# Optimization experiments

Hardware: AMD Instinct MI355X
Metric: run time of the kernel (lower is better)

Reference implementation:

```python
import jax, jax.numpy as jnp
import numpy as np

D_MODEL = 1024
N_HEADS = 16
D_HEAD = D_MODEL // N_HEADS


def setup_inputs() -> dict:
    key = jax.random.key(0)
    ks = jax.random.split(key, 9)
    s = 1.0 / np.sqrt(D_MODEL)
    x = jax.random.normal(ks[0], (2, 2048, D_MODEL), dtype=jnp.float32)
    Wq = jax.random.uniform(ks[1], (D_MODEL, D_MODEL), jnp.float32, -s, s)
    bq = jax.random.uniform(ks[2], (D_MODEL,), jnp.float32, -s, s)
    Wk = jax.random.uniform(ks[3], (D_MODEL, D_MODEL), jnp.float32, -s, s)
    bk = jax.random.uniform(ks[4], (D_MODEL,), jnp.float32, -s, s)
    Wv = jax.random.uniform(ks[5], (D_MODEL, D_MODEL), jnp.float32, -s, s)
    bv = jax.random.uniform(ks[6], (D_MODEL,), jnp.float32, -s, s)
    Wo = jax.random.uniform(ks[7], (D_MODEL, D_MODEL), jnp.float32, -s, s)
    bo = jax.random.uniform(ks[8], (D_MODEL,), jnp.float32, -s, s)
    return {"x": x, "Wq": Wq, "bq": bq, "Wk": Wk, "bk": bk,
            "Wv": Wv, "bv": bv, "Wo": Wo, "bo": bo}


def reference(x, Wq, bq, Wk, bk, Wv, bv, Wo, bo):
    B, T, _ = x.shape
    # projections: (B, T, d_model) -> (B, H, T, d_head)
    def split_heads(y):
        return y.reshape(B, T, N_HEADS, D_HEAD).transpose(0, 2, 1, 3)
    Q = split_heads(x @ Wq + bq)
    K = split_heads(x @ Wk + bk)
    V = split_heads(x @ Wv + bv)
    scores = jnp.einsum('bhqd,bhkd->bhqk', Q, K) / jnp.sqrt(jnp.float32(D_HEAD))
    causal = jnp.tril(jnp.ones((T, T), dtype=bool))  # allowed positions
    scores = jnp.where(causal, scores, -jnp.inf)
    attn = jax.nn.softmax(scores, axis=-1)
    out = jnp.einsum('bhqk,bhkd->bhqd', attn, V)
    out = out.transpose(0, 2, 1, 3).reshape(B, T, D_MODEL)
    return out @ Wo + bo
```

## Files before the change

kernel.cpp:

```cpp
#include <hip/hip_runtime.h>

typedef unsigned short u16;
typedef unsigned int u32;

#define DM 1024
#define NH 16
#define DH 64
#define BB 2
#define TT 2048

#define SCLQ 0.18033688f

using frag8  = __attribute__((ext_vector_type(8))) short;
using bf16x8 = __attribute__((ext_vector_type(8))) __bf16;
using f32x4  = __attribute__((ext_vector_type(4))) float;

__device__ inline u16 f2bf(float f) {
  union { float f; u32 u; } v; v.f = f;
  u32 r = v.u + 0x7fffu + ((v.u >> 16) & 1u);
  return (u16)(r >> 16);
}

__device__ inline f32x4 mfma_bf16(frag8 a, frag8 b, f32x4 c) {
  return __builtin_amdgcn_mfma_f32_16x16x32_bf16(
      __builtin_bit_cast(bf16x8, a), __builtin_bit_cast(bf16x8, b), c, 0, 0, 0);
}

__device__ inline void gld16(void* lds, const void* g) {
  __builtin_amdgcn_global_load_lds(
      (const __attribute__((address_space(1))) void*)g,
      (__attribute__((address_space(3))) void*)lds, 16, 0, 0);
}

__device__ inline int swi(int row, int chunk) {
  return row * 64 + ((chunk ^ (row & 7)) << 3);
}

__global__ __launch_bounds__(256) void cvt_x_kernel(const float* __restrict__ X,
                                                    u16* __restrict__ Y) {
  int i = blockIdx.x * 256 + threadIdx.x;
  float4 v = ((const float4*)X)[i];
  ushort4 o;
  o.x = f2bf(v.x); o.y = f2bf(v.y); o.z = f2bf(v.z); o.w = f2bf(v.w);
  ((ushort4*)Y)[i] = o;
}

__global__ __launch_bounds__(256) void transpose_w_kernel(
    const float* __restrict__ W0, const float* __restrict__ W1,
    const float* __restrict__ W2, const float* __restrict__ W3,
    u16* __restrict__ O0, u16* __restrict__ O1,
    u16* __restrict__ O2, u16* __restrict__ O3) {
  const float* W; u16* Ot;
  switch (blockIdx.z) {
    case 0: W = W0; Ot = O0; break;
    case 1: W = W1; Ot = O1; break;
    case 2: W = W2; Ot = O2; break;
    default: W = W3; Ot = O3; break;
  }
  __shared__ u16 Ls[64][72];
  int tid = threadIdx.x;
  int n0 = blockIdx.x * 64;
  int k0 = blockIdx.y * 64;
#pragma unroll
  for (int p = 0; p < 4; ++p) {
    int id = tid + p * 256;
    int row = id >> 4;
    int c4 = (id & 15) * 4;
    float4 v = *(const float4*)&W[(size_t)(k0 + row) * DM + n0 + c4];
    ushort4 o; o.x = f2bf(v.x); o.y = f2bf(v.y); o.z = f2bf(v.z); o.w = f2bf(v.w);
    *(ushort4*)&Ls[row][c4] = o;
  }
  __syncthreads();
#pragma unroll
  for (int p = 0; p < 4; ++p) {
    int id = tid + p * 256;
    int row = id >> 4;
    int c4 = (id & 15) * 4;
    ushort4 o;
    o.x = Ls[c4 + 0][row]; o.y = Ls[c4 + 1][row];
    o.z = Ls[c4 + 2][row]; o.w = Ls[c4 + 3][row];
    *(ushort4*)&Ot[(size_t)(n0 + row) * DM + k0 + c4] = o;
  }
}

__global__ __launch_bounds__(256, 3) void gemm_qkv_kernel(
    const u16* __restrict__ A, const u16* __restrict__ Bt,
    const float* __restrict__ b0, const float* __restrict__ b1,
    const float* __restrict__ b2,
    u16* __restrict__ QK, u16* __restrict__ Vb) {
  constexpr int K = 1024;
  __shared__ u16 As[2][4096];
  __shared__ u16 Bs[2][4096];
  int tid = threadIdx.x;
  int lane = tid & 63, w = tid >> 6;
  int qd = lane >> 4, ln = lane & 15;
  int wm = (w & 1) * 64, wn = (w >> 1) * 64;
  int m0 = blockIdx.y * 128, n0 = blockIdx.x * 128;
  f32x4 z = {0.f, 0.f, 0.f, 0.f};
  f32x4 acc[4][4];
#pragma unroll
  for (int mi = 0; mi < 4; ++mi)
#pragma unroll
    for (int ni = 0; ni < 4; ++ni) acc[mi][ni] = z;

  const u16* ga = A + (size_t)(m0 + w * 32 + (lane >> 2)) * K + (lane & 3) * 8;
  const u16* gb = Bt + (size_t)(n0 + w * 32 + (lane >> 2)) * K + (lane & 3) * 8;

  gld16(&As[0][w * 1024],       ga);
  gld16(&As[0][w * 1024 + 512], ga + 16 * K);
  gld16(&Bs[0][w * 1024],       gb);
  gld16(&Bs[0][w * 1024 + 512], gb + 16 * K);

  for (int k0 = 0; k0 < K; k0 += 32) {
    int cur = (k0 >> 5) & 1;
    __syncthreads();
    if (k0 + 32 < K) {
      int nb = cur ^ 1;
      gld16(&As[nb][w * 1024],       ga + k0 + 32);
      gld16(&As[nb][w * 1024 + 512], ga + k0 + 32 + 16 * K);
      gld16(&Bs[nb][w * 1024],       gb + k0 + 32);
      gld16(&Bs[nb][w * 1024 + 512], gb + k0 + 32 + 16 * K);
    }
    frag8 af[4], bfr[4];
#pragma unroll
    for (int mi = 0; mi < 4; ++mi)
      af[mi] = *(const frag8*)&As[cur][(wm + mi * 16 + ln) * 32 + qd * 8];
#pragma unroll
    for (int ni = 0; ni < 4; ++ni)
      bfr[ni] = *(const frag8*)&Bs[cur][(wn + ni * 16 + ln) * 32 + qd * 8];
#pragma unroll
    for (int mi = 0; mi < 4; ++mi)
#pragma unroll
      for (int ni = 0; ni < 4; ++ni)
        acc[mi][ni] = mfma_bf16(af[mi], bfr[ni], acc[mi][ni]);
  }

#pragma unroll
  for (int ni = 0; ni < 4; ++ni) {
    int col = n0 + wn + ni * 16 + ln;
    if (col < 2048) {
      bool isq = col < 1024;
      float bias = isq ? b0[col] : b1[col - 1024];
#pragma unroll
      for (int mi = 0; mi < 4; ++mi) {
        int row = m0 + wm + mi * 16 + qd * 4;
#pragma unroll
        for (int r = 0; r < 4; ++r) {
          float v = acc[mi][ni][r] + bias;
          if (isq) v *= SCLQ;
          QK[(size_t)(row + r) * 2048 + col] = f2bf(v);
        }
      }
    } else {
      int c2 = col - 2048;
      float bias = b2[c2];
#pragma unroll
      for (int mi = 0; mi < 4; ++mi) {
        int row = m0 + wm + mi * 16 + qd * 4;
#pragma unroll
        for (int r = 0; r < 4; ++r)
          Vb[(size_t)(row + r) * 1024 + c2] = f2bf(acc[mi][ni][r] + bias);
      }
    }
  }
}

__global__ __launch_bounds__(256) void gemm_out_kernel(
    const u16* __restrict__ A, const u16* __restrict__ Bt,
    const float* __restrict__ b0, float* __restrict__ Cf) {
  constexpr int K = 1024;
  __shared__ u16 As[2][4096];
  __shared__ u16 Bs[2][2048];
  int tid = threadIdx.x;
  int lane = tid & 63, w = tid >> 6;
  int qd = lane >> 4, ln = lane & 15;
  int m0 = blockIdx.y * 128, n0 = blockIdx.x * 64;
  f32x4 z = {0.f, 0.f, 0.f, 0.f};
  f32x4 acc[2][4];
#pragma unroll
  for (int mi = 0; mi < 2; ++mi)
#pragma unroll
    for (int ni = 0; ni < 4; ++ni) acc[mi][ni] = z;

  const u16* ga = A + (size_t)(m0 + w * 32 + (lane >> 2)) * K + (lane & 3) * 8;
  const u16* gb = Bt + (size_t)(n0 + w * 16 + (lane >> 2)) * K + (lane & 3) * 8;

  gld16(&As[0][w * 1024],       ga);
  gld16(&As[0][w * 1024 + 512], ga + 16 * K);
  gld16(&Bs[0][w * 512],        gb);

  for (int k0 = 0; k0 < K; k0 += 32) {
    int cur = (k0 >> 5) & 1;
    __syncthreads();
    if (k0 + 32 < K) {
      int nb = cur ^ 1;
      gld16(&As[nb][w * 1024],       ga + k0 + 32);
      gld16(&As[nb][w * 1024 + 512], ga + k0 + 32 + 16 * K);
      gld16(&Bs[nb][w * 512],        gb + k0 + 32);
    }
    frag8 af[2], bfr[4];
#pragma unroll
    for (int mi = 0; mi < 2; ++mi)
      af[mi] = *(const frag8*)&As[cur][(w * 32 + mi * 16 + ln) * 32 + qd * 8];
#pragma unroll
    for (int ni = 0; ni < 4; ++ni)
      bfr[ni] = *(const frag8*)&Bs[cur][(ni * 16 + ln) * 32 + qd * 8];
#pragma unroll
    for (int mi = 0; mi < 2; ++mi)
#pragma unroll
      for (int ni = 0; ni < 4; ++ni)
        acc[mi][ni] = mfma_bf16(af[mi], bfr[ni], acc[mi][ni]);
  }

#pragma unroll
  for (int ni = 0; ni < 4; ++ni) {
    int col = n0 + ni * 16 + ln;
    float bias = b0[col];
#pragma unroll
    for (int mi = 0; mi < 2; ++mi) {
      int row = m0 + w * 32 + mi * 16 + qd * 4;
#pragma unroll
      for (int r = 0; r < 4; ++r)
        Cf[(size_t)(row + r) * 1024 + col] = acc[mi][ni][r] + bias;
    }
  }
}

__global__ __launch_bounds__(256) void transpose_v_kernel(const u16* __restrict__ V,
                                                          u16* __restrict__ Vt) {
  int bh = blockIdx.y;
  int b = bh >> 4, h = bh & 15;
  int t0 = blockIdx.x * 64;
  __shared__ u16 Ls[64][72];
  int tid = threadIdx.x;
#pragma unroll
  for (int p = 0; p < 2; ++p) {
    int id = tid + p * 256;
    int row = id >> 3, seg = id & 7;
    *(uint4*)&Ls[row][seg * 8] =
        *(const uint4*)&V[(size_t)(b * TT + t0 + row) * DM + h * DH + seg * 8];
  }
  __syncthreads();
#pragma unroll
  for (int p = 0; p < 2; ++p) {
    int id = tid + p * 256;
    int d = id >> 3, seg = id & 7;
    union { u16 s[8]; uint4 v; } tmp;
#pragma unroll
    for (int j = 0; j < 8; ++j) tmp.s[j] = Ls[seg * 8 + j][d];
    *(uint4*)&Vt[(size_t)(bh * DH + d) * TT + t0 + seg * 8] = tmp.v;
  }
}

__global__ __launch_bounds__(256, 4) void flash5_kernel(const u16* __restrict__ QK,
                                                        const u16* __restrict__ Vt,
                                                        u16* __restrict__ O) {
  int qt = blockIdx.x;
  int bh = blockIdx.y;
  int b = bh >> 4, h = bh & 15;
  int q0 = qt * 64;
  __shared__ u16 Ks[2 * 4096];
  __shared__ u16 Vs[2 * 4096];
  __shared__ u16 Ps[4096];
  int tid = threadIdx.x;
  int lane = tid & 63, w = tid >> 6;
  int qd = lane >> 4, ln = lane & 15;

  frag8 qf[2];
#pragma unroll
  for (int kk = 0; kk < 2; ++kk)
    qf[kk] = *(const frag8*)&QK[(size_t)(b * TT + q0 + w * 16 + ln) * 2048 +
                                h * 64 + kk * 32 + qd * 8];

  int lr = lane >> 3, lc = (lane & 7) ^ lr;
  const u16* Kg  = &QK[(size_t)(b * TT + w * 16 + lr) * 2048 + 1024 + h * 64 + lc * 8];
  const u16* Kg2 = Kg + 8 * 2048;
  const u16* Vg  = &Vt[(size_t)(bh * 64 + w * 16 + lr) * 2048 + lc * 8];
  const u16* Vg2 = Vg + 8 * 2048;
  int ldsw = w * 1024;

  int nkt = qt + 1;

  gld16(&Ks[ldsw],       Kg);
  gld16(&Ks[ldsw + 512], Kg2);
  gld16(&Vs[ldsw],       Vg);
  gld16(&Vs[ldsw + 512], Vg2);

  float l = 0.f;
  f32x4 z = {0.f, 0.f, 0.f, 0.f};
  f32x4 o[4] = {z, z, z, z};

  for (int kt = 0; kt < nkt; ++kt) {
    int cur = kt & 1;
    int cb = cur * 4096;
    __syncthreads();

    if (kt + 1 < nkt) {
      int nb = (cur ^ 1) * 4096;
      size_t ko = (size_t)(kt + 1) * 64 * 2048;
      int vo = (kt + 1) * 64;
      gld16(&Ks[nb + ldsw],       Kg + ko);
      gld16(&Ks[nb + ldsw + 512], Kg2 + ko);
      gld16(&Vs[nb + ldsw],       Vg + vo);
      gld16(&Vs[nb + ldsw + 512], Vg2 + vo);
    }

    bool diag = (kt == qt);

    f32x4 s[4] = {z, z, z, z};
    __builtin_amdgcn_s_setprio(1);
#pragma unroll
    for (int mi = 0; mi < 4; ++mi) {
      if (diag && mi > w) continue;
#pragma unroll
      for (int kk = 0; kk < 2; ++kk) {
        frag8 ak = *(const frag8*)&Ks[cb + swi(mi * 16 + ln, 4 * kk + qd)];
        s[mi] = mfma_bf16(ak, qf[kk], s[mi]);
      }
    }
    __builtin_amdgcn_s_setprio(0);

#pragma unroll
    for (int mi = 0; mi < 4; ++mi) {
      int pb = swi(w * 16 + ln, 2 * mi + (qd >> 1)) + (qd & 1) * 4;
      if (diag && mi > w) {
        uint2 zz; zz.x = 0u; zz.y = 0u;
        *(uint2*)&Ps[pb] = zz;
        continue;
      }
      float p0 = __builtin_amdgcn_exp2f(s[mi][0]);
      float p1 = __builtin_amdgcn_exp2f(s[mi][1]);
      float p2 = __builtin_amdgcn_exp2f(s[mi][2]);
      float p3 = __builtin_amdgcn_exp2f(s[mi][3]);
      if (diag && mi == w) {
        p0 = (qd * 4 + 0 <= ln) ? p0 : 0.f;
        p1 = (qd * 4 + 1 <= ln) ? p1 : 0.f;
        p2 = (qd * 4 + 2 <= ln) ? p2 : 0.f;
        p3 = (qd * 4 + 3 <= ln) ? p3 : 0.f;
      }
      l += (p0 + p1) + (p2 + p3);
      u32 u0 = __builtin_bit_cast(u32, p0) + 0x8000u;
      u32 u1 = __builtin_bit_cast(u32, p1) + 0x8000u;
      u32 u2 = __builtin_bit_cast(u32, p2) + 0x8000u;
      u32 u3 = __builtin_bit_cast(u32, p3) + 0x8000u;
      uint2 pk;
      pk.x = __builtin_amdgcn_perm(u1, u0, 0x07060302u);
      pk.y = __builtin_amdgcn_perm(u3, u2, 0x07060302u);
      *(uint2*)&Ps[pb] = pk;
    }

    __builtin_amdgcn_s_setprio(1);
#pragma unroll
    for (int kk = 0; kk < 2; ++kk) {
      if (diag && kk == 1 && w < 2) continue;
      frag8 bp = *(const frag8*)&Ps[swi(w * 16 + ln, 4 * kk + qd)];
#pragma unroll
      for (int mi = 0; mi < 4; ++mi) {
        frag8 av = *(const frag8*)&Vs[cb + swi(mi * 16 + ln, 4 * kk + qd)];
        o[mi] = mfma_bf16(av, bp, o[mi]);
      }
    }
    __builtin_amdgcn_s_setprio(0);
  }

  l += __shfl_xor(l, 16);
  l += __shfl_xor(l, 32);
  float rl = 1.0f / l;

#pragma unroll
  for (int mi = 0; mi < 4; ++mi) {
    ushort4 ov;
    ov.x = f2bf(o[mi][0] * rl); ov.y = f2bf(o[mi][1] * rl);
    ov.z = f2bf(o[mi][2] * rl); ov.w = f2bf(o[mi][3] * rl);
    *(ushort4*)&O[(size_t)(b * TT + q0 + w * 16 + ln) * DM + h * 64 + mi * 16 + qd * 4] = ov;
  }
}

extern "C" void kernel_launch(void* const* d_in, const int* in_sizes, int n_in,
                              void* d_out, int out_size, void* d_ws, size_t ws_size,
                              hipStream_t stream) {
  const float* x  = (const float*)d_in[0];
  const float* Wq = (const float*)d_in[1];
  const float* bq = (const float*)d_in[2];
  const float* Wk = (const float*)d_in[3];
  const float* bk = (const float*)d_in[4];
  const float* Wv = (const float*)d_in[5];
  const float* bv = (const float*)d_in[6];
  const float* Wo = (const float*)d_in[7];
  const float* bo = (const float*)d_in[8];

  char* ws = (char*)d_ws;
  const size_t MB = 1ull << 20;
  u16* xbf  = (u16*)(ws + 0);
  u16* Wcat = (u16*)(ws + 8 * MB);
  u16* Wot  = (u16*)(ws + 14 * MB);
  u16* QKb  = (u16*)(ws + 16 * MB);
  u16* Vbb  = (u16*)(ws + 32 * MB);
  u16* Vtb  = (u16*)(ws + 40 * MB);
  u16* Ob   = (u16*)(ws + 48 * MB);

  cvt_x_kernel<<<4096, 256, 0, stream>>>(x, xbf);
  transpose_w_kernel<<<dim3(16, 16, 4), 256, 0, stream>>>(
      Wq, Wk, Wv, Wo, Wcat, Wcat + 1024 * 1024, Wcat + 2 * 1024 * 1024, Wot);
  gemm_qkv_kernel<<<dim3(24, 32), 256, 0, stream>>>(
      xbf, Wcat, bq, bk, bv, QKb, Vbb);
  transpose_v_kernel<<<dim3(32, 32), 256, 0, stream>>>(Vbb, Vtb);
  flash5_kernel<<<dim3(32, 32), 256, 0, stream>>>(QKb, Vtb, Ob);
  gemm_out_kernel<<<dim3(16, 32), 256, 0, stream>>>(Ob, Wot, bo, (float*)d_out);
}
```

Measured before the change: 211.7 us.

## Fuse V transpose into QKV GEMM epilogue and reorder flash block schedule

The QKV GEMM epilogue now stages output tiles in shared memory through a swizzled layout and writes coalesced 16-byte rows. For V columns it writes the transposed layout directly, which removes the separate transpose_v kernel and its extra global round trip. The flash kernel remaps block indices so heads are grouped together and query-tile order alternates, to balance causal work and improve K/V cache locality. The cost is an extra LDS pass and barrier in the GEMM epilogue.

New measurement: 185.0 us. 12.6% less time.

```diff
diff --git a/kernel.cpp b/kernel.cpp
--- a/kernel.cpp
+++ b/kernel.cpp
@@ -34,6 +34,10 @@
 
 __device__ inline int swi(int row, int chunk) {
   return row * 64 + ((chunk ^ (row & 7)) << 3);
+}
+
+__device__ inline int sidx128(int row, int col) {
+  return row * 128 + ((((col >> 3) ^ (row & 7)) << 3) | (col & 7));
 }
 
 __global__ __launch_bounds__(256) void cvt_x_kernel(const float* __restrict__ X,
@@ -87,10 +91,11 @@
     const u16* __restrict__ A, const u16* __restrict__ Bt,
     const float* __restrict__ b0, const float* __restrict__ b1,
     const float* __restrict__ b2,
-    u16* __restrict__ QK, u16* __restrict__ Vb) {
+    u16* __restrict__ QK, u16* __restrict__ Vt) {
   constexpr int K = 1024;
-  __shared__ u16 As[2][4096];
-  __shared__ u16 Bs[2][4096];
+  __shared__ u16 sm[16384];
+  u16* As = sm;
+  u16* Bs = sm + 8192;
   int tid = threadIdx.x;
   int lane = tid & 63, w = tid >> 6;
   int qd = lane >> 4, ln = lane & 15;
@@ -106,28 +111,28 @@
   const u16* ga = A + (size_t)(m0 + w * 32 + (lane >> 2)) * K + (lane & 3) * 8;
   const u16* gb = Bt + (size_t)(n0 + w * 32 + (lane >> 2)) * K + (lane & 3) * 8;
 
-  gld16(&As[0][w * 1024],       ga);
-  gld16(&As[0][w * 1024 + 512], ga + 16 * K);
-  gld16(&Bs[0][w * 1024],       gb);
-  gld16(&Bs[0][w * 1024 + 512], gb + 16 * K);
+  gld16(&As[w * 1024],       ga);
+  gld16(&As[w * 1024 + 512], ga + 16 * K);
+  gld16(&Bs[w * 1024],       gb);
+  gld16(&Bs[w * 1024 + 512], gb + 16 * K);
 
   for (int k0 = 0; k0 < K; k0 += 32) {
     int cur = (k0 >> 5) & 1;
     __syncthreads();
     if (k0 + 32 < K) {
       int nb = cur ^ 1;
-      gld16(&As[nb][w * 1024],       ga + k0 + 32);
-      gld16(&As[nb][w * 1024 + 512], ga + k0 + 32 + 16 * K);
-      gld16(&Bs[nb][w * 1024],       gb + k0 + 32);
-      gld16(&Bs[nb][w * 1024 + 512], gb + k0 + 32 + 16 * K);
+      gld16(&As[nb * 4096 + w * 1024],       ga + k0 + 32);
+      gld16(&As[nb * 4096 + w * 1024 + 512], ga + k0 + 32 + 16 * K);
+      gld16(&Bs[nb * 4096 + w * 1024],       gb + k0 + 32);
+      gld16(&Bs[nb * 4096 + w * 1024 + 512], gb + k0 + 32 + 16 * K);
     }
     frag8 af[4], bfr[4];
 #pragma unroll
     for (int mi = 0; mi < 4; ++mi)
-      af[mi] = *(const frag8*)&As[cur][(wm + mi * 16 + ln) * 32 + qd * 8];
+      af[mi] = *(const frag8*)&As[cur * 4096 + (wm + mi * 16 + ln) * 32 + qd * 8];
 #pragma unroll
     for (int ni = 0; ni < 4; ++ni)
-      bfr[ni] = *(const frag8*)&Bs[cur][(wn + ni * 16 + ln) * 32 + qd * 8];
+      bfr[ni] = *(const frag8*)&Bs[cur * 4096 + (wn + ni * 16 + ln) * 32 + qd * 8];
 #pragma unroll
     for (int mi = 0; mi < 4; ++mi)
 #pragma unroll
@@ -135,32 +140,58 @@
         acc[mi][ni] = mfma_bf16(af[mi], bfr[ni], acc[mi][ni]);
   }
 
-#pragma unroll
-  for (int ni = 0; ni < 4; ++ni) {
-    int col = n0 + wn + ni * 16 + ln;
-    if (col < 2048) {
-      bool isq = col < 1024;
+  __syncthreads();
+
+  if (n0 < 2048) {
+    bool isq = (n0 < 1024);
+#pragma unroll
+    for (int ni = 0; ni < 4; ++ni) {
+      int c_loc = wn + ni * 16 + ln;
+      int col = n0 + c_loc;
       float bias = isq ? b0[col] : b1[col - 1024];
 #pragma unroll
       for (int mi = 0; mi < 4; ++mi) {
-        int row = m0 + wm + mi * 16 + qd * 4;
+        int rbase = wm + mi * 16 + qd * 4;
 #pragma unroll
         for (int r = 0; r < 4; ++r) {
           float v = acc[mi][ni][r] + bias;
           if (isq) v *= SCLQ;
-          QK[(size_t)(row + r) * 2048 + col] = f2bf(v);
+          sm[sidx128(rbase + r, c_loc)] = f2bf(v);
         }
       }
-    } else {
-      int c2 = col - 2048;
-      float bias = b2[c2];
+    }
+    __syncthreads();
+#pragma unroll
+    for (int p = 0; p < 8; ++p) {
+      int id = p * 256 + tid;
+      int tr = id >> 4, cr = id & 15;
+      uint4 v = *(const uint4*)&sm[tr * 128 + ((cr ^ (tr & 7)) << 3)];
+      *(uint4*)&QK[(size_t)(m0 + tr) * 2048 + n0 + cr * 8] = v;
+    }
+  } else {
+    int b = m0 >> 11, tb = m0 & 2047;
+    int n0v = n0 - 2048;
+#pragma unroll
+    for (int ni = 0; ni < 4; ++ni) {
+      int c_loc = wn + ni * 16 + ln;
+      float bias = b2[n0v + c_loc];
 #pragma unroll
       for (int mi = 0; mi < 4; ++mi) {
-        int row = m0 + wm + mi * 16 + qd * 4;
-#pragma unroll
-        for (int r = 0; r < 4; ++r)
-          Vb[(size_t)(row + r) * 1024 + c2] = f2bf(acc[mi][ni][r] + bias);
-      }
+        int tbase = wm + mi * 16 + qd * 4;
+        u32 lo = ((u32)f2bf(acc[mi][ni][1] + bias) << 16) | f2bf(acc[mi][ni][0] + bias);
+        u32 hi = ((u32)f2bf(acc[mi][ni][3] + bias) << 16) | f2bf(acc[mi][ni][2] + bias);
+        uint2 pk; pk.x = lo; pk.y = hi;
+        int idx = c_loc * 128 + ((((tbase >> 3) ^ (c_loc & 7)) << 3) | (tbase & 7));
+        *(uint2*)&sm[idx] = pk;
+      }
+    }
+    __syncthreads();
+#pragma unroll
+    for (int p = 0; p < 8; ++p) {
+      int id = p * 256 + tid;
+      int d_loc = id >> 4, tc = id & 15;
+      uint4 v = *(const uint4*)&sm[d_loc * 128 + ((tc ^ (d_loc & 7)) << 3)];
+      *(uint4*)&Vt[(size_t)(b * 1024 + n0v + d_loc) * 2048 + tb + tc * 8] = v;
     }
   }
 }
@@ -226,37 +257,13 @@
   }
 }
 
-__global__ __launch_bounds__(256) void transpose_v_kernel(const u16* __restrict__ V,
-                                                          u16* __restrict__ Vt) {
-  int bh = blockIdx.y;
-  int b = bh >> 4, h = bh & 15;
-  int t0 = blockIdx.x * 64;
-  __shared__ u16 Ls[64][72];
-  int tid = threadIdx.x;
-#pragma unroll
-  for (int p = 0; p < 2; ++p) {
-    int id = tid + p * 256;
-    int row = id >> 3, seg = id & 7;
-    *(uint4*)&Ls[row][seg * 8] =
-        *(const uint4*)&V[(size_t)(b * TT + t0 + row) * DM + h * DH + seg * 8];
-  }
-  __syncthreads();
-#pragma unroll
-  for (int p = 0; p < 2; ++p) {
-    int id = tid + p * 256;
-    int d = id >> 3, seg = id & 7;
-    union { u16 s[8]; uint4 v; } tmp;
-#pragma unroll
-    for (int j = 0; j < 8; ++j) tmp.s[j] = Ls[seg * 8 + j][d];
-    *(uint4*)&Vt[(size_t)(bh * DH + d) * TT + t0 + seg * 8] = tmp.v;
-  }
-}
-
-__global__ __launch_bounds__(256, 4) void flash5_kernel(const u16* __restrict__ QK,
+__global__ __launch_bounds__(256, 4) void flash6_kernel(const u16* __restrict__ QK,
                                                         const u16* __restrict__ Vt,
                                                         u16* __restrict__ O) {
-  int qt = blockIdx.x;
-  int bh = blockIdx.y;
+  int lin = blockIdx.y * 32 + blockIdx.x;
+  int rr = lin >> 8, cc = lin & 255;
+  int bh = (rr << 3) | (cc >> 5);
+  int qt = (rr & 1) ? (31 - (cc & 31)) : (cc & 31);
   int b = bh >> 4, h = bh & 15;
   int q0 = qt * 64;
   __shared__ u16 Ks[2 * 4096];
@@ -395,7 +402,6 @@
   u16* Wcat = (u16*)(ws + 8 * MB);
   u16* Wot  = (u16*)(ws + 14 * MB);
   u16* QKb  = (u16*)(ws + 16 * MB);
-  u16* Vbb  = (u16*)(ws + 32 * MB);
   u16* Vtb  = (u16*)(ws + 40 * MB);
   u16* Ob   = (u16*)(ws + 48 * MB);
 
@@ -403,8 +409,7 @@
   transpose_w_kernel<<<dim3(16, 16, 4), 256, 0, stream>>>(
       Wq, Wk, Wv, Wo, Wcat, Wcat + 1024 * 1024, Wcat + 2 * 1024 * 1024, Wot);
   gemm_qkv_kernel<<<dim3(24, 32), 256, 0, stream>>>(
-      xbf, Wcat, bq, bk, bv, QKb, Vbb);
-  transpose_v_kernel<<<dim3(32, 32), 256, 0, stream>>>(Vbb, Vtb);
-  flash5_kernel<<<dim3(32, 32), 256, 0, stream>>>(QKb, Vtb, Ob);
+      xbf, Wcat, bq, bk, bv, QKb, Vtb);
+  flash6_kernel<<<dim3(32, 32), 256, 0, stream>>>(QKb, Vtb, Ob);
   gemm_out_kernel<<<dim3(16, 32), 256, 0, stream>>>(Ob, Wot, bo, (float*)d_out);
 }
```
